# Optimization experiments

Measured on AMD Instinct MI355X. Metric: run time of the kernel, lower is better.

The kernel has to match this reference:

```python
import jax, jax.numpy as jnp
import numpy as np

B, N, DIM = 2, 2048, 1024
HEADS, DIM_HEAD = 16, 64
SOFTCAP = 50.0
ROPE_THETA = 10000.0


def setup_inputs() -> dict:
    key = jax.random.key(0)
    k1, k2, k3 = jax.random.split(key, 3)
    x = jax.random.normal(k1, (B, N, DIM), jnp.float32)
    # structured modality positions: (type, offset, length), non-overlapping, in-bounds
    mods = np.zeros((B, 4, 3), np.int64)
    base_offsets = [200, 700, 1200, 1700]
    for b in range(B):
        for m, o in enumerate(base_offsets):
            mods[b, m] = (0, o + b * 16, 256)
    modalities = jnp.asarray(mods)
    gamma = jnp.zeros((DIM,), jnp.float32)           # RMSNorm gamma (init zeros, used as gamma+1)
    w_qkv = jax.random.normal(k2, (DIM, 3 * HEADS * DIM_HEAD), jnp.float32) * 0.02
    w_out = jax.random.normal(k3, (HEADS * DIM_HEAD, DIM), jnp.float32) * 0.02
    return {"x": x, "modalities": modalities, "gamma": gamma, "w_qkv": w_qkv, "w_out": w_out}


def _rotate_half(x):
    # interleaved-pair rotation, matching rotary-embedding-torch default
    x1, x2 = x[..., 0::2], x[..., 1::2]
    return jnp.stack((-x2, x1), axis=-1).reshape(x.shape)


def reference(x, modalities, gamma, w_qkv, w_out):
    b, n, d = x.shape
    h, dh = HEADS, DIM_HEAD
    seq = jnp.arange(n)
    off = modalities[..., 1]      # [b, m]
    length = modalities[..., 2]   # [b, m]

    # --- modality-aware rotary positions (span interior shrunk by offset [1, -1]) ---
    in_span = (seq[None, None, :] >= (off + 1)[:, :, None]) & (seq[None, None, :] < (off + length)[:, :, None])
    is_any_modality = in_span.any(axis=1)                                   # [b, n]
    pos = (seq[None, :] - jnp.cumsum(is_any_modality.astype(jnp.int32), axis=-1)).astype(jnp.float32)

    # --- RMSNorm: l2norm(x) * sqrt(d) * (gamma + 1) ---
    norm = jnp.maximum(jnp.sqrt(jnp.sum(x * x, axis=-1, keepdims=True)), 1e-12)
    xn = x / norm * jnp.sqrt(jnp.float32(d)) * (gamma + 1.0)

    # --- qkv projection, split heads -> [b, h, n, dh] ---
    qkv = (xn @ w_qkv).reshape(b, n, 3, h, dh)
    q, k, v = jnp.moveaxis(qkv, 2, 0)        # each [b, n, h, dh]
    q = jnp.transpose(q, (0, 2, 1, 3))
    k = jnp.transpose(k, (0, 2, 1, 3))
    v = jnp.transpose(v, (0, 2, 1, 3))

    # --- rotary embedding with modality-aware positions ---
    inv_freq = ROPE_THETA ** (-jnp.arange(0, dh, 2, dtype=jnp.float32) / dh)  # [dh/2]
    ang = pos[:, None, :, None] * inv_freq                                    # [b, 1, n, dh/2]
    ang = jnp.repeat(ang, 2, axis=-1)                                         # [b, 1, n, dh]
    cos, sin = jnp.cos(ang), jnp.sin(ang)
    q = q * cos + _rotate_half(q) * sin
    k = k * cos + _rotate_half(k) * sin

    # --- transfusion attention mask: causal OR per-modality bidirectional span ---
    causal_mask = seq[:, None] >= seq[None, :]                                 # [n, n]
    q_ge = seq[None, None, :] >= off[:, :, None]                               # [b, m, n]
    kv_lt = seq[None, None, :] < (off + length)[:, :, None]                    # [b, m, n]
    mod_mask = (q_ge[:, :, :, None] & kv_lt[:, :, None, :]).any(axis=1)        # [b, n, n]
    mask = causal_mask[None] | mod_mask                                        # [b, n, n]

    # --- attention with softclamp(50) ---
    scale = dh ** -0.5
    sim = jnp.einsum('bhid,bhjd->bhij', q, k) * scale
    sim = jnp.tanh(sim / SOFTCAP) * SOFTCAP
    sim = jnp.where(mask[:, None], sim, jnp.finfo(sim.dtype).min)
    attn = jax.nn.softmax(sim, axis=-1)
    out = jnp.einsum('bhij,bhjd->bhid', attn, v)                               # [b, h, n, dh]
    out = jnp.transpose(out, (0, 2, 1, 3)).reshape(b, n, h * dh)
    return out @ w_out
```

## Files before the change

kernel.cpp:

```cpp
#include <hip/hip_runtime.h>
#include <hip/hip_bf16.h>
#include <stdint.h>

#define B_ 2
#define N_ 2048
#define H_ 16
#define DIM_ 1024
#define NH3 3072
#define ROWS (B_*N_)
#define BHN (B_*H_*N_)

typedef __attribute__((ext_vector_type(8))) short bf16x8;
typedef __attribute__((ext_vector_type(4))) float f32x4;
typedef unsigned short u16;

__device__ __forceinline__ u16 f2bf(float f){
  union { float f; uint32_t u; } v; v.f = f;
  return (u16)((v.u + 0x7fffu + ((v.u >> 16) & 1u)) >> 16);
}

#if __has_builtin(__builtin_amdgcn_exp2f)
#define EXP2F(x) __builtin_amdgcn_exp2f(x)
#else
#define EXP2F(x) __expf((x) * 0.6931471805599453f)
#endif
#if __has_builtin(__builtin_amdgcn_rcpf)
#define RCPF(x) __builtin_amdgcn_rcpf(x)
#else
#define RCPF(x) (1.0f / (x))
#endif

#define GLL16(g, l) __builtin_amdgcn_global_load_lds( \
    (const __attribute__((address_space(1))) void*)(g), \
    (__attribute__((address_space(3))) void*)(l), 16, 0, 0)

__global__ __launch_bounds__(256) void k_prep(
    const float* __restrict__ x, const float* __restrict__ gamma,
    const float* __restrict__ wqkv, const float* __restrict__ wout,
    const int* __restrict__ mods,
    u16* __restrict__ xn, u16* __restrict__ wqkvT, u16* __restrict__ woutT,
    float* __restrict__ cosT, float* __restrict__ sinT)
{
  __shared__ float tile[32][33];
  const int bx = blockIdx.x;
  const int tid = threadIdx.x;
  if (bx < 4096){
    const int row = bx;
    const float4 xv = ((const float4*)(x + (size_t)row*DIM_))[tid];
    float ss = xv.x*xv.x + xv.y*xv.y + xv.z*xv.z + xv.w*xv.w;
#pragma unroll
    for (int d = 1; d < 64; d <<= 1) ss += __shfl_xor(ss, d);
    if ((tid & 63) == 0) tile[1][tid >> 6] = ss;
    __syncthreads();
    float tot = tile[1][0] + tile[1][1] + tile[1][2] + tile[1][3];
    float scl = 32.0f / fmaxf(sqrtf(tot), 1e-12f);
    const float4 gv = ((const float4*)gamma)[tid];
    ushort4 o;
    o.x = f2bf(xv.x * scl * (gv.x + 1.0f));
    o.y = f2bf(xv.y * scl * (gv.y + 1.0f));
    o.z = f2bf(xv.z * scl * (gv.z + 1.0f));
    o.w = f2bf(xv.w * scl * (gv.w + 1.0f));
    ((ushort4*)(xn + (size_t)row*DIM_))[tid] = o;
  } else if (bx < 8192){
    const int t = bx - 4096;
    const int bxx = t & 127, by = t >> 7;
    const float* src; u16* dst; int C, bc;
    if (bxx < 96){ src = wqkv; dst = wqkvT; C = NH3;  bc = bxx*32; }
    else         { src = wout; dst = woutT; C = DIM_; bc = (bxx-96)*32; }
    const int R = DIM_;
    const int tx = tid & 31, ty = tid >> 5;
    const int br = by * 32;
#pragma unroll
    for (int i = 0; i < 32; i += 8)
      tile[ty + i][tx] = src[(size_t)(br + ty + i)*C + bc + tx];
    __syncthreads();
#pragma unroll
    for (int i = 0; i < 32; i += 8)
      dst[(size_t)(bc + ty + i)*R + br + tx] = f2bf(tile[tx][ty + i]);
  } else {
    const int t = (bx - 8192)*256 + tid;
    const int f = t & 31, bn = t >> 5;
    const int b = bn >> 11, n = bn & (N_-1);
    int cum = 0;
#pragma unroll
    for (int m = 0; m < 4; ++m){
      const int off = mods[(b*4 + m)*3 + 1];
      const int len = mods[(b*4 + m)*3 + 2];
      cum += min(max(n - off, 0), len - 1);
    }
    const float pos = (float)(n - cum);
    const float inv = powf(10000.0f, -(float)(2*f) / 64.0f);
    float s, c;
    sincosf(pos * inv, &s, &c);
    cosT[t] = c; sinT[t] = s;
  }
}

template<int MODE, int BM>
__global__ __launch_bounds__(256) void k_gemm(
    const u16* __restrict__ A, const u16* __restrict__ Bt,
    int K, int Nc,
    float* __restrict__ outf,
    const float* __restrict__ cosT, const float* __restrict__ sinT,
    u16* __restrict__ qo, u16* __restrict__ ko, u16* __restrict__ vt)
{
  constexpr int MR = BM/32;
  constexpr int RA = BM/8;
  constexpr int CNT = (RA + 16)/4;
  __shared__ u16 lA[BM*64];
  __shared__ u16 lB[128*64];
  const int tid = threadIdx.x;
  const int wid = tid >> 6, lane = tid & 63;
  const int nx = gridDim.x;
  const int orig = blockIdx.y * nx + blockIdx.x;
  const int qq = (nx * gridDim.y) >> 3;
  const int wgid = (orig & 7) * qq + (orig >> 3);
  const int m0 = (wgid % nx) * BM, n0 = (wgid / nx) * 128;
  const int wm = wid >> 1, wn = wid & 1;
  const int srow = lane >> 3, sch = lane & 7;
  const int r16 = lane & 15, g4 = lane >> 4;
  f32x4 acc[MR][4] = {};
  const int ksteps = K >> 6;
  for (int kt = 0; kt < ksteps; ++kt){
    const int kb = kt*64;
    const int gch = sch ^ srow;
#pragma unroll
    for (int i = 0; i < CNT; ++i){
      const int reg = wid*CNT + i;
      if (reg < RA){
        const int row = reg*8 + srow;
        GLL16(A + (size_t)(m0 + row)*K + kb + gch*8, &lA[reg*512]);
      } else {
        const int r2 = reg - RA;
        const int row = r2*8 + srow;
        GLL16(Bt + (size_t)(n0 + row)*K + kb + gch*8, &lB[r2*512]);
      }
    }
    __syncthreads();
#pragma unroll
    for (int t = 0; t < 2; ++t){
      bf16x8 af[MR], bfr[4];
#pragma unroll
      for (int m = 0; m < MR; ++m){
        int row = wm*(BM/2) + m*16 + r16;
        int ch = (t*4 + g4) ^ (r16 & 7);
        af[m] = *(const bf16x8*)&lA[row*64 + ch*8];
      }
#pragma unroll
      for (int n = 0; n < 4; ++n){
        int row = wn*64 + n*16 + r16;
        int ch = (t*4 + g4) ^ (r16 & 7);
        bfr[n] = *(const bf16x8*)&lB[row*64 + ch*8];
      }
#pragma unroll
      for (int m = 0; m < MR; ++m)
#pragma unroll
        for (int n = 0; n < 4; ++n)
          acc[m][n] = __builtin_amdgcn_mfma_f32_16x16x32_bf16(af[m], bfr[n], acc[m][n], 0, 0, 0);
    }
    __syncthreads();
  }
#pragma unroll
  for (int m = 0; m < MR; ++m){
#pragma unroll
    for (int n = 0; n < 4; ++n){
      if constexpr (MODE == 0){
        const int gcol = n0 + wn*64 + n*16 + r16;
        const int s3 = gcol >> 10, hh = (gcol >> 6) & 15, d = gcol & 63;
        const int grow0 = m0 + wm*(BM/2) + m*16 + g4*4;
        const int b = grow0 >> 11, nn0 = grow0 & (N_-1);
        const size_t hb = (size_t)(b*H_ + hh);
        if (s3 == 2){
          uint32_t w01, w23;
          asm("v_cvt_pk_bf16_f32 %0, %1, %2" : "=v"(w01) : "v"(acc[m][n][0]), "v"(acc[m][n][1]));
          asm("v_cvt_pk_bf16_f32 %0, %1, %2" : "=v"(w23) : "v"(acc[m][n][2]), "v"(acc[m][n][3]));
          *reinterpret_cast<uint2*>(&vt[(hb*64 + d)*N_ + nn0]) = make_uint2(w01, w23);
        } else {
#pragma unroll
          for (int r = 0; r < 4; ++r){
            const float v = acc[m][n][r];
            const float part = __shfl_xor(v, 1);
            const int nn = nn0 + r;
            const int pidx = (b*N_ + nn)*32 + (d >> 1);
            const float c = cosT[pidx], sn = sinT[pidx];
            const float rot = (d & 1) ? (v*c + part*sn) : (v*c - part*sn);
            const u16 val = f2bf(rot);
            if (s3 == 0) qo[(hb*N_ + nn)*64 + d] = val;
            else         ko[(hb*N_ + nn)*64 + d] = val;
          }
        }
      } else {
#pragma unroll
        for (int r = 0; r < 4; ++r){
          const int grow = m0 + wm*(BM/2) + m*16 + g4*4 + r;
          const int gcol = n0 + wn*64 + n*16 + r16;
          outf[(size_t)grow*Nc + gcol] = acc[m][n][r];
        }
      }
    }
  }
}

#define PST 68
__global__ __launch_bounds__(512) void k_attn(
    const u16* __restrict__ qb, const u16* __restrict__ kb, const u16* __restrict__ vt,
    const int* __restrict__ mods, u16* __restrict__ xo)
{
  __shared__ u16 lK[64*64];
  __shared__ u16 lV[64*64];
  __shared__ u16 lP[8*16*PST];
  const int tid = threadIdx.x, wid = tid >> 6, lane = tid & 63;
  const int id = blockIdx.x;
  const int xcd = id & 7, rank = id >> 3;
  const int bh = xcd + 8*(rank & 3);
  const int qslot = rank >> 2;
  const int tp = (qslot < 8) ? (15 - qslot) : (qslot - 8);
  const int b = bh >> 4, h = bh & 15;
  const int r16 = lane & 15, g4 = lane >> 4;
  const int srow = lane >> 3, sch = lane & 7;
  int moff[4], mend[4];
#pragma unroll
  for (int m = 0; m < 4; ++m){
    moff[m] = mods[(b*4+m)*3+1];
    mend[m] = moff[m] + mods[(b*4+m)*3+2];
  }
  const u16* kbase = kb + (size_t)bh*N_*64;
  const u16* vbase = vt + (size_t)bh*64*N_;
  u16* lPw = &lP[wid*16*PST];

  const int q0 = tp*128 + wid*16;
  const int i  = q0 + r16;
  const int imax = tp*128 + 127;
  int jmax = 0, jmax0 = 0;
#pragma unroll
  for (int m = 0; m < 4; ++m){
    if (i  >= moff[m]) jmax  = max(jmax,  mend[m]);
    if (q0 >= moff[m]) jmax0 = max(jmax0, mend[m]);
  }
  const int thrmin = max(q0, jmax0 - 1);
  const u16* qrow = qb + ((size_t)bh*N_ + q0 + r16)*64;
  const bf16x8 aq0 = *(const bf16x8*)&qrow[g4*8];
  const bf16x8 aq1 = *(const bf16x8*)&qrow[32 + g4*8];
  f32x4 o[4] = {};
  f32x4 acc_s = {};
  bf16x8 ones;
#pragma unroll
  for (int j = 0; j < 8; ++j) ones[j] = (short)0x3F80;

  const float D1 = 0.18033688011112043f;
  const float D3 = -3.7570183356483704e-07f;

  for (int kt = 0; kt < N_/64; ++kt){
    bool proc = (kt*64 <= imax);
    if (!proc){
#pragma unroll
      for (int m = 0; m < 4; ++m)
        if (imax >= moff[m] && kt*64 < mend[m]) proc = true;
    }
    if (!proc) continue;
    __syncthreads();
    {
      const int gch = sch ^ srow;
      GLL16(kbase + (size_t)(kt*64 + wid*8 + srow)*64 + gch*8, &lK[wid*512]);
      GLL16(vbase + (size_t)(wid*8 + srow)*N_ + kt*64 + gch*8, &lV[wid*512]);
    }
    __syncthreads();
    f32x4 s[4] = {};
    __builtin_amdgcn_s_setprio(1);
#pragma unroll
    for (int cb = 0; cb < 4; ++cb){
#pragma unroll
      for (int t = 0; t < 2; ++t){
        int row = cb*16 + r16;
        int ch = (t*4 + g4) ^ (row & 7);
        bf16x8 bk = *(const bf16x8*)&lK[row*64 + ch*8];
        s[cb] = __builtin_amdgcn_mfma_f32_16x16x32_bf16(bk, t ? aq1 : aq0, s[cb], 0, 0, 0);
      }
    }
    __builtin_amdgcn_s_setprio(0);
    const int thr = max(i, jmax - 1) - kt*64;
    const bool nomask = (kt*64 + 63 <= thrmin);
#pragma unroll
    for (int cb = 0; cb < 4; ++cb){
      float p[4];
#pragma unroll
      for (int r = 0; r < 4; ++r){
        const float sv = s[cb][r];
        const float w = sv*sv;
        p[r] = EXP2F(sv * fmaf(w, D3, D1));
      }
      if (!nomask){
#pragma unroll
        for (int r = 0; r < 4; ++r)
          p[r] = (cb*16 + g4*4 + r <= thr) ? p[r] : 0.0f;
      }
      uint32_t w01, w23;
      asm("v_cvt_pk_bf16_f32 %0, %1, %2" : "=v"(w01) : "v"(p[0]), "v"(p[1]));
      asm("v_cvt_pk_bf16_f32 %0, %1, %2" : "=v"(w23) : "v"(p[2]), "v"(p[3]));
      *reinterpret_cast<uint2*>(&lPw[r16*PST + cb*16 + g4*4]) = make_uint2(w01, w23);
    }
    asm volatile("s_waitcnt lgkmcnt(0)" ::: "memory");
    __builtin_amdgcn_sched_barrier(0);
    union { uint2 h[2]; bf16x8 v; } u0, u1;
    u0.h[0] = *(const uint2*)&lPw[r16*PST + g4*8];
    u0.h[1] = *(const uint2*)&lPw[r16*PST + g4*8 + 4];
    u1.h[0] = *(const uint2*)&lPw[r16*PST + 32 + g4*8];
    u1.h[1] = *(const uint2*)&lPw[r16*PST + 32 + g4*8 + 4];
    __builtin_amdgcn_s_setprio(1);
    acc_s = __builtin_amdgcn_mfma_f32_16x16x32_bf16(u0.v, ones, acc_s, 0, 0, 0);
    acc_s = __builtin_amdgcn_mfma_f32_16x16x32_bf16(u1.v, ones, acc_s, 0, 0, 0);
#pragma unroll
    for (int cb = 0; cb < 4; ++cb){
#pragma unroll
      for (int t = 0; t < 2; ++t){
        int d = cb*16 + r16;
        int ch = (t*4 + g4) ^ (d & 7);
        bf16x8 bv = *(const bf16x8*)&lV[d*64 + ch*8];
        o[cb] = __builtin_amdgcn_mfma_f32_16x16x32_bf16(t ? u1.v : u0.v, bv, o[cb], 0, 0, 0);
      }
    }
    __builtin_amdgcn_s_setprio(0);
  }
#pragma unroll
  for (int r = 0; r < 4; ++r){
    const float linv = RCPF(acc_s[r]);
    const int iq = q0 + g4*4 + r;
#pragma unroll
    for (int cb = 0; cb < 4; ++cb)
      xo[(size_t)(b*N_ + iq)*DIM_ + h*64 + cb*16 + r16] = f2bf(o[cb][r]*linv);
  }
}

extern "C" void kernel_launch(void* const* d_in, const int* in_sizes, int n_in,
                              void* d_out, int out_size, void* d_ws, size_t ws_size,
                              hipStream_t stream){
  const float* x     = (const float*)d_in[0];
  const int*   mods  = (const int*)d_in[1];
  const float* gamma = (const float*)d_in[2];
  const float* wqkv  = (const float*)d_in[3];
  const float* wout  = (const float*)d_in[4];
  float* outp = (float*)d_out;

  char* p = (char*)d_ws;
  auto alloc = [&](size_t bytes) -> char* {
    char* r = p; p += (bytes + 255) & ~(size_t)255; return r;
  };
  float* cosT  = (float*)alloc((size_t)B_*N_*32*4);
  float* sinT  = (float*)alloc((size_t)B_*N_*32*4);
  u16* wqkvT   = (u16*)alloc((size_t)NH3*DIM_*2);
  u16* woutT   = (u16*)alloc((size_t)DIM_*DIM_*2);
  u16* xn      = (u16*)alloc((size_t)ROWS*DIM_*2);
  u16* qbb     = (u16*)alloc((size_t)BHN*64*2);
  u16* kbb     = (u16*)alloc((size_t)BHN*64*2);
  u16* vtb     = (u16*)alloc((size_t)BHN*64*2);
  u16* xo      = (u16*)alloc((size_t)ROWS*DIM_*2);

  k_prep<<<8704, 256, 0, stream>>>(x, gamma, wqkv, wout, mods, xn, wqkvT, woutT, cosT, sinT);
  k_gemm<0,128><<<dim3(ROWS/128, NH3/128), 256, 0, stream>>>(xn, wqkvT, DIM_, NH3, nullptr, cosT, sinT, qbb, kbb, vtb);
  k_attn<<<512, 512, 0, stream>>>(qbb, kbb, vtb, mods, xo);
  k_gemm<1,64><<<dim3(ROWS/64, DIM_/128), 256, 0, stream>>>(xo, woutT, DIM_, DIM_, outp, nullptr, nullptr, nullptr, nullptr, nullptr);
}
```

Baseline: 115.9 us.

## Give each attention wave two 16-row query tiles to reuse K/V fragments

The attention block shrinks from 8 waves to 4, and each wave now handles 32 query rows as two 16-row halves. Each K and V fragment read from LDS feeds two MFMAs, which halves LDS read traffic per unit of work. Each wave now issues two global-to-LDS loads per tile. The cost is higher register pressure from doubled accumulators and fewer waves per block to hide latency.

Result: slower. 130.5 us (+12.6%).

```diff
diff --git a/kernel.cpp b/kernel.cpp
--- a/kernel.cpp
+++ b/kernel.cpp
@@ -202,13 +202,13 @@
 }
 
 #define PST 68
-__global__ __launch_bounds__(512) void k_attn(
+__global__ __launch_bounds__(256) void k_attn(
     const u16* __restrict__ qb, const u16* __restrict__ kb, const u16* __restrict__ vt,
     const int* __restrict__ mods, u16* __restrict__ xo)
 {
   __shared__ u16 lK[64*64];
   __shared__ u16 lV[64*64];
-  __shared__ u16 lP[8*16*PST];
+  __shared__ u16 lP[4*32*PST];
   const int tid = threadIdx.x, wid = tid >> 6, lane = tid & 63;
   const int id = blockIdx.x;
   const int xcd = id & 7, rank = id >> 3;
@@ -226,23 +226,28 @@
   }
   const u16* kbase = kb + (size_t)bh*N_*64;
   const u16* vbase = vt + (size_t)bh*64*N_;
-  u16* lPw = &lP[wid*16*PST];
-
-  const int q0 = tp*128 + wid*16;
-  const int i  = q0 + r16;
+  u16* lPw = &lP[wid*32*PST];
+
+  const int q0 = tp*128 + wid*32;
+  const int iA = q0 + r16;
+  const int iB = q0 + 16 + r16;
   const int imax = tp*128 + 127;
-  int jmax = 0, jmax0 = 0;
+  int jmaxA = 0, jmaxB = 0, jmax0 = 0;
 #pragma unroll
   for (int m = 0; m < 4; ++m){
-    if (i  >= moff[m]) jmax  = max(jmax,  mend[m]);
+    if (iA >= moff[m]) jmaxA = max(jmaxA, mend[m]);
+    if (iB >= moff[m]) jmaxB = max(jmaxB, mend[m]);
     if (q0 >= moff[m]) jmax0 = max(jmax0, mend[m]);
   }
   const int thrmin = max(q0, jmax0 - 1);
-  const u16* qrow = qb + ((size_t)bh*N_ + q0 + r16)*64;
-  const bf16x8 aq0 = *(const bf16x8*)&qrow[g4*8];
-  const bf16x8 aq1 = *(const bf16x8*)&qrow[32 + g4*8];
-  f32x4 o[4] = {};
-  f32x4 acc_s = {};
+  const u16* qrowA = qb + ((size_t)bh*N_ + iA)*64;
+  const u16* qrowB = qb + ((size_t)bh*N_ + iB)*64;
+  const bf16x8 aqA0 = *(const bf16x8*)&qrowA[g4*8];
+  const bf16x8 aqA1 = *(const bf16x8*)&qrowA[32 + g4*8];
+  const bf16x8 aqB0 = *(const bf16x8*)&qrowB[g4*8];
+  const bf16x8 aqB1 = *(const bf16x8*)&qrowB[32 + g4*8];
+  f32x4 oA[4] = {}, oB[4] = {};
+  f32x4 acc_sA = {}, acc_sB = {};
   bf16x8 ones;
 #pragma unroll
   for (int j = 0; j < 8; ++j) ones[j] = (short)0x3F80;
@@ -261,11 +266,15 @@
     __syncthreads();
     {
       const int gch = sch ^ srow;
-      GLL16(kbase + (size_t)(kt*64 + wid*8 + srow)*64 + gch*8, &lK[wid*512]);
-      GLL16(vbase + (size_t)(wid*8 + srow)*N_ + kt*64 + gch*8, &lV[wid*512]);
-    }
-    __syncthreads();
-    f32x4 s[4] = {};
+#pragma unroll
+      for (int ld = 0; ld < 2; ++ld){
+        const int reg = wid*2 + ld;
+        GLL16(kbase + (size_t)(kt*64 + reg*8 + srow)*64 + gch*8, &lK[reg*512]);
+        GLL16(vbase + (size_t)(reg*8 + srow)*N_ + kt*64 + gch*8, &lV[reg*512]);
+      }
+    }
+    __syncthreads();
+    f32x4 s0[4] = {}, s1[4] = {};
     __builtin_amdgcn_s_setprio(1);
 #pragma unroll
     for (int cb = 0; cb < 4; ++cb){
@@ -274,41 +283,54 @@
         int row = cb*16 + r16;
         int ch = (t*4 + g4) ^ (row & 7);
         bf16x8 bk = *(const bf16x8*)&lK[row*64 + ch*8];
-        s[cb] = __builtin_amdgcn_mfma_f32_16x16x32_bf16(bk, t ? aq1 : aq0, s[cb], 0, 0, 0);
+        s0[cb] = __builtin_amdgcn_mfma_f32_16x16x32_bf16(bk, t ? aqA1 : aqA0, s0[cb], 0, 0, 0);
+        s1[cb] = __builtin_amdgcn_mfma_f32_16x16x32_bf16(bk, t ? aqB1 : aqB0, s1[cb], 0, 0, 0);
       }
     }
     __builtin_amdgcn_s_setprio(0);
-    const int thr = max(i, jmax - 1) - kt*64;
+    const int thrA = max(iA, jmaxA - 1) - kt*64;
+    const int thrB = max(iB, jmaxB - 1) - kt*64;
     const bool nomask = (kt*64 + 63 <= thrmin);
 #pragma unroll
-    for (int cb = 0; cb < 4; ++cb){
-      float p[4];
-#pragma unroll
-      for (int r = 0; r < 4; ++r){
-        const float sv = s[cb][r];
-        const float w = sv*sv;
-        p[r] = EXP2F(sv * fmaf(w, D3, D1));
-      }
-      if (!nomask){
-#pragma unroll
-        for (int r = 0; r < 4; ++r)
-          p[r] = (cb*16 + g4*4 + r <= thr) ? p[r] : 0.0f;
-      }
-      uint32_t w01, w23;
-      asm("v_cvt_pk_bf16_f32 %0, %1, %2" : "=v"(w01) : "v"(p[0]), "v"(p[1]));
-      asm("v_cvt_pk_bf16_f32 %0, %1, %2" : "=v"(w23) : "v"(p[2]), "v"(p[3]));
-      *reinterpret_cast<uint2*>(&lPw[r16*PST + cb*16 + g4*4]) = make_uint2(w01, w23);
+    for (int half = 0; half < 2; ++half){
+      const f32x4* sH = half ? s1 : s0;
+      const int thr = half ? thrB : thrA;
+#pragma unroll
+      for (int cb = 0; cb < 4; ++cb){
+        float p[4];
+#pragma unroll
+        for (int r = 0; r < 4; ++r){
+          const float sv = sH[cb][r];
+          const float w = sv*sv;
+          p[r] = EXP2F(sv * fmaf(w, D3, D1));
+        }
+        if (!nomask){
+#pragma unroll
+          for (int r = 0; r < 4; ++r)
+            p[r] = (cb*16 + g4*4 + r <= thr) ? p[r] : 0.0f;
+        }
+        uint32_t w01, w23;
+        asm("v_cvt_pk_bf16_f32 %0, %1, %2" : "=v"(w01) : "v"(p[0]), "v"(p[1]));
+        asm("v_cvt_pk_bf16_f32 %0, %1, %2" : "=v"(w23) : "v"(p[2]), "v"(p[3]));
+        *reinterpret_cast<uint2*>(&lPw[(half*16 + r16)*PST + cb*16 + g4*4]) = make_uint2(w01, w23);
+      }
     }
     asm volatile("s_waitcnt lgkmcnt(0)" ::: "memory");
     __builtin_amdgcn_sched_barrier(0);
-    union { uint2 h[2]; bf16x8 v; } u0, u1;
-    u0.h[0] = *(const uint2*)&lPw[r16*PST + g4*8];
-    u0.h[1] = *(const uint2*)&lPw[r16*PST + g4*8 + 4];
-    u1.h[0] = *(const uint2*)&lPw[r16*PST + 32 + g4*8];
-    u1.h[1] = *(const uint2*)&lPw[r16*PST + 32 + g4*8 + 4];
+    union { uint2 hh[2]; bf16x8 v; } a0, a1, b0, b1;
+    a0.hh[0] = *(const uint2*)&lPw[r16*PST + g4*8];
+    a0.hh[1] = *(const uint2*)&lPw[r16*PST + g4*8 + 4];
+    a1.hh[0] = *(const uint2*)&lPw[r16*PST + 32 + g4*8];
+    a1.hh[1] = *(const uint2*)&lPw[r16*PST + 32 + g4*8 + 4];
+    b0.hh[0] = *(const uint2*)&lPw[(16 + r16)*PST + g4*8];
+    b0.hh[1] = *(const uint2*)&lPw[(16 + r16)*PST + g4*8 + 4];
+    b1.hh[0] = *(const uint2*)&lPw[(16 + r16)*PST + 32 + g4*8];
+    b1.hh[1] = *(const uint2*)&lPw[(16 + r16)*PST + 32 + g4*8 + 4];
     __builtin_amdgcn_s_setprio(1);
-    acc_s = __builtin_amdgcn_mfma_f32_16x16x32_bf16(u0.v, ones, acc_s, 0, 0, 0);
-    acc_s = __builtin_amdgcn_mfma_f32_16x16x32_bf16(u1.v, ones, acc_s, 0, 0, 0);
+    acc_sA = __builtin_amdgcn_mfma_f32_16x16x32_bf16(a0.v, ones, acc_sA, 0, 0, 0);
+    acc_sA = __builtin_amdgcn_mfma_f32_16x16x32_bf16(a1.v, ones, acc_sA, 0, 0, 0);
+    acc_sB = __builtin_amdgcn_mfma_f32_16x16x32_bf16(b0.v, ones, acc_sB, 0, 0, 0);
+    acc_sB = __builtin_amdgcn_mfma_f32_16x16x32_bf16(b1.v, ones, acc_sB, 0, 0, 0);
 #pragma unroll
     for (int cb = 0; cb < 4; ++cb){
 #pragma unroll
@@ -316,18 +338,23 @@
         int d = cb*16 + r16;
         int ch = (t*4 + g4) ^ (d & 7);
         bf16x8 bv = *(const bf16x8*)&lV[d*64 + ch*8];
-        o[cb] = __builtin_amdgcn_mfma_f32_16x16x32_bf16(t ? u1.v : u0.v, bv, o[cb], 0, 0, 0);
+        oA[cb] = __builtin_amdgcn_mfma_f32_16x16x32_bf16(t ? a1.v : a0.v, bv, oA[cb], 0, 0, 0);
+        oB[cb] = __builtin_amdgcn_mfma_f32_16x16x32_bf16(t ? b1.v : b0.v, bv, oB[cb], 0, 0, 0);
       }
     }
     __builtin_amdgcn_s_setprio(0);
   }
 #pragma unroll
   for (int r = 0; r < 4; ++r){
-    const float linv = RCPF(acc_s[r]);
-    const int iq = q0 + g4*4 + r;
-#pragma unroll
-    for (int cb = 0; cb < 4; ++cb)
-      xo[(size_t)(b*N_ + iq)*DIM_ + h*64 + cb*16 + r16] = f2bf(o[cb][r]*linv);
+    const float linvA = RCPF(acc_sA[r]);
+    const float linvB = RCPF(acc_sB[r]);
+    const int iqA = q0 + g4*4 + r;
+    const int iqB = q0 + 16 + g4*4 + r;
+#pragma unroll
+    for (int cb = 0; cb < 4; ++cb){
+      xo[(size_t)(b*N_ + iqA)*DIM_ + h*64 + cb*16 + r16] = f2bf(oA[cb][r]*linvA);
+      xo[(size_t)(b*N_ + iqB)*DIM_ + h*64 + cb*16 + r16] = f2bf(oB[cb][r]*linvB);
+    }
   }
 }
 
@@ -357,6 +384,6 @@
 
   k_prep<<<8704, 256, 0, stream>>>(x, gamma, wqkv, wout, mods, xn, wqkvT, woutT, cosT, sinT);
   k_gemm<0,128><<<dim3(ROWS/128, NH3/128), 256, 0, stream>>>(xn, wqkvT, DIM_, NH3, nullptr, cosT, sinT, qbb, kbb, vtb);
-  k_attn<<<512, 512, 0, stream>>>(qbb, kbb, vtb, mods, xo);
+  k_attn<<<512, 256, 0, stream>>>(qbb, kbb, vtb, mods, xo);
   k_gemm<1,64><<<dim3(ROWS/64, DIM_/128), 256, 0, stream>>>(xo, woutT, DIM_, DIM_, outp, nullptr, nullptr, nullptr, nullptr, nullptr);
 }
```

## Switch attention to 32x32 MFMA with register-resident P via permlane swap

Applied to the files above, without the earlier changes.

Rewrites the attention inner loop to use 32x32x16 bf16 MFMA tiles, so each of 4 waves handles 32 query rows instead of 8 waves each handling 16. The P matrix is kept in registers and rearranged with v_permlane32_swap instead of a round trip through LDS, and the row sum is accumulated in scalar registers instead of a ones-matrix MFMA. This aims to remove LDS traffic, the waitcnt barrier and extra MFMA work per tile. The cost is higher register pressure and half the threads per block, which lowers occupancy and latency hiding.

New measurement: 128.9 us. 1.11x slower.

```diff
diff --git a/kernel.cpp b/kernel.cpp
--- a/kernel.cpp
+++ b/kernel.cpp
@@ -12,6 +12,7 @@
 
 typedef __attribute__((ext_vector_type(8))) short bf16x8;
 typedef __attribute__((ext_vector_type(4))) float f32x4;
+typedef __attribute__((ext_vector_type(16))) float f32x16;
 typedef unsigned short u16;
 
 __device__ __forceinline__ u16 f2bf(float f){
@@ -201,14 +202,12 @@
   }
 }
 
-#define PST 68
-__global__ __launch_bounds__(512) void k_attn(
+__global__ __launch_bounds__(256) void k_attn(
     const u16* __restrict__ qb, const u16* __restrict__ kb, const u16* __restrict__ vt,
     const int* __restrict__ mods, u16* __restrict__ xo)
 {
   __shared__ u16 lK[64*64];
   __shared__ u16 lV[64*64];
-  __shared__ u16 lP[8*16*PST];
   const int tid = threadIdx.x, wid = tid >> 6, lane = tid & 63;
   const int id = blockIdx.x;
   const int xcd = id & 7, rank = id >> 3;
@@ -216,7 +215,7 @@
   const int qslot = rank >> 2;
   const int tp = (qslot < 8) ? (15 - qslot) : (qslot - 8);
   const int b = bh >> 4, h = bh & 15;
-  const int r16 = lane & 15, g4 = lane >> 4;
+  const int l31 = lane & 31, hi = lane >> 5;
   const int srow = lane >> 3, sch = lane & 7;
   int moff[4], mend[4];
 #pragma unroll
@@ -226,26 +225,26 @@
   }
   const u16* kbase = kb + (size_t)bh*N_*64;
   const u16* vbase = vt + (size_t)bh*64*N_;
-  u16* lPw = &lP[wid*16*PST];
-
-  const int q0 = tp*128 + wid*16;
-  const int i  = q0 + r16;
+
+  const int q0w = tp*128 + wid*32;
+  const int qG  = q0w + l31;
   const int imax = tp*128 + 127;
   int jmax = 0, jmax0 = 0;
 #pragma unroll
   for (int m = 0; m < 4; ++m){
-    if (i  >= moff[m]) jmax  = max(jmax,  mend[m]);
-    if (q0 >= moff[m]) jmax0 = max(jmax0, mend[m]);
-  }
-  const int thrmin = max(q0, jmax0 - 1);
-  const u16* qrow = qb + ((size_t)bh*N_ + q0 + r16)*64;
-  const bf16x8 aq0 = *(const bf16x8*)&qrow[g4*8];
-  const bf16x8 aq1 = *(const bf16x8*)&qrow[32 + g4*8];
-  f32x4 o[4] = {};
-  f32x4 acc_s = {};
-  bf16x8 ones;
-#pragma unroll
-  for (int j = 0; j < 8; ++j) ones[j] = (short)0x3F80;
+    if (qG  >= moff[m]) jmax  = max(jmax,  mend[m]);
+    if (q0w >= moff[m]) jmax0 = max(jmax0, mend[m]);
+  }
+  const int thrg = max(qG, jmax - 1);
+  const int thrmin = max(q0w, jmax0 - 1);
+  const u16* qrow = qb + ((size_t)bh*N_ + qG)*64;
+  bf16x8 qf[4];
+#pragma unroll
+  for (int t = 0; t < 4; ++t)
+    qf[t] = *(const bf16x8*)&qrow[t*16 + hi*8];
+
+  f32x16 o0 = {}, o1 = {};
+  float lsum = 0.f;
 
   const float D1 = 0.18033688011112043f;
   const float D3 = -3.7570183356483704e-07f;
@@ -261,73 +260,83 @@
     __syncthreads();
     {
       const int gch = sch ^ srow;
-      GLL16(kbase + (size_t)(kt*64 + wid*8 + srow)*64 + gch*8, &lK[wid*512]);
-      GLL16(vbase + (size_t)(wid*8 + srow)*N_ + kt*64 + gch*8, &lV[wid*512]);
-    }
-    __syncthreads();
-    f32x4 s[4] = {};
+#pragma unroll
+      for (int ld = 0; ld < 2; ++ld){
+        const int reg = wid*2 + ld;
+        GLL16(kbase + (size_t)(kt*64 + reg*8 + srow)*64 + gch*8, &lK[reg*512]);
+        GLL16(vbase + (size_t)(reg*8 + srow)*N_ + kt*64 + gch*8, &lV[reg*512]);
+      }
+    }
+    __syncthreads();
+    f32x16 s0 = {}, s1 = {};
     __builtin_amdgcn_s_setprio(1);
 #pragma unroll
-    for (int cb = 0; cb < 4; ++cb){
-#pragma unroll
-      for (int t = 0; t < 2; ++t){
-        int row = cb*16 + r16;
-        int ch = (t*4 + g4) ^ (row & 7);
-        bf16x8 bk = *(const bf16x8*)&lK[row*64 + ch*8];
-        s[cb] = __builtin_amdgcn_mfma_f32_16x16x32_bf16(bk, t ? aq1 : aq0, s[cb], 0, 0, 0);
-      }
+    for (int t = 0; t < 4; ++t){
+      const int c = t*2 + hi;
+      const int r0 = l31, r1 = 32 + l31;
+      const bf16x8 k0 = *(const bf16x8*)&lK[r0*64 + (c ^ (r0 & 7))*8];
+      const bf16x8 k1 = *(const bf16x8*)&lK[r1*64 + (c ^ (r1 & 7))*8];
+      s0 = __builtin_amdgcn_mfma_f32_32x32x16_bf16(k0, qf[t], s0, 0, 0, 0);
+      s1 = __builtin_amdgcn_mfma_f32_32x32x16_bf16(k1, qf[t], s1, 0, 0, 0);
     }
     __builtin_amdgcn_s_setprio(0);
-    const int thr = max(i, jmax - 1) - kt*64;
+    const int thr = thrg - kt*64;
     const bool nomask = (kt*64 + 63 <= thrmin);
-#pragma unroll
-    for (int cb = 0; cb < 4; ++cb){
-      float p[4];
-#pragma unroll
-      for (int r = 0; r < 4; ++r){
-        const float sv = s[cb][r];
+    float p0[16], p1[16];
+#pragma unroll
+    for (int reg = 0; reg < 16; ++reg){
+      const int kb32 = (reg & 3) + 8*(reg >> 2);
+      {
+        const float sv = s0[reg];
         const float w = sv*sv;
-        p[r] = EXP2F(sv * fmaf(w, D3, D1));
-      }
-      if (!nomask){
-#pragma unroll
-        for (int r = 0; r < 4; ++r)
-          p[r] = (cb*16 + g4*4 + r <= thr) ? p[r] : 0.0f;
-      }
-      uint32_t w01, w23;
-      asm("v_cvt_pk_bf16_f32 %0, %1, %2" : "=v"(w01) : "v"(p[0]), "v"(p[1]));
-      asm("v_cvt_pk_bf16_f32 %0, %1, %2" : "=v"(w23) : "v"(p[2]), "v"(p[3]));
-      *reinterpret_cast<uint2*>(&lPw[r16*PST + cb*16 + g4*4]) = make_uint2(w01, w23);
-    }
-    asm volatile("s_waitcnt lgkmcnt(0)" ::: "memory");
-    __builtin_amdgcn_sched_barrier(0);
-    union { uint2 h[2]; bf16x8 v; } u0, u1;
-    u0.h[0] = *(const uint2*)&lPw[r16*PST + g4*8];
-    u0.h[1] = *(const uint2*)&lPw[r16*PST + g4*8 + 4];
-    u1.h[0] = *(const uint2*)&lPw[r16*PST + 32 + g4*8];
-    u1.h[1] = *(const uint2*)&lPw[r16*PST + 32 + g4*8 + 4];
+        float p = EXP2F(sv * fmaf(w, D3, D1));
+        if (!nomask) p = (kb32 + 4*hi <= thr) ? p : 0.0f;
+        p0[reg] = p; lsum += p;
+      }
+      {
+        const float sv = s1[reg];
+        const float w = sv*sv;
+        float p = EXP2F(sv * fmaf(w, D3, D1));
+        if (!nomask) p = (32 + kb32 + 4*hi <= thr) ? p : 0.0f;
+        p1[reg] = p; lsum += p;
+      }
+    }
+    bf16x8 pf[4];
+#pragma unroll
+    for (int ks = 0; ks < 4; ++ks){
+      const float* pp = (ks < 2) ? p0 : p1;
+      const int q32 = ks & 1;
+      uint32_t X0, X1, Y0, Y1;
+      asm("v_cvt_pk_bf16_f32 %0, %1, %2" : "=v"(X0) : "v"(pp[q32*8+0]), "v"(pp[q32*8+1]));
+      asm("v_cvt_pk_bf16_f32 %0, %1, %2" : "=v"(X1) : "v"(pp[q32*8+2]), "v"(pp[q32*8+3]));
+      asm("v_cvt_pk_bf16_f32 %0, %1, %2" : "=v"(Y0) : "v"(pp[q32*8+4]), "v"(pp[q32*8+5]));
+      asm("v_cvt_pk_bf16_f32 %0, %1, %2" : "=v"(Y1) : "v"(pp[q32*8+6]), "v"(pp[q32*8+7]));
+      asm volatile("v_permlane32_swap_b32 %0, %1" : "+v"(X0), "+v"(Y0));
+      asm volatile("v_permlane32_swap_b32 %0, %1" : "+v"(X1), "+v"(Y1));
+      union { uint32_t d[4]; bf16x8 v; } u;
+      u.d[0] = X0; u.d[1] = X1; u.d[2] = Y0; u.d[3] = Y1;
+      pf[ks] = u.v;
+    }
     __builtin_amdgcn_s_setprio(1);
-    acc_s = __builtin_amdgcn_mfma_f32_16x16x32_bf16(u0.v, ones, acc_s, 0, 0, 0);
-    acc_s = __builtin_amdgcn_mfma_f32_16x16x32_bf16(u1.v, ones, acc_s, 0, 0, 0);
-#pragma unroll
-    for (int cb = 0; cb < 4; ++cb){
-#pragma unroll
-      for (int t = 0; t < 2; ++t){
-        int d = cb*16 + r16;
-        int ch = (t*4 + g4) ^ (d & 7);
-        bf16x8 bv = *(const bf16x8*)&lV[d*64 + ch*8];
-        o[cb] = __builtin_amdgcn_mfma_f32_16x16x32_bf16(t ? u1.v : u0.v, bv, o[cb], 0, 0, 0);
-      }
+#pragma unroll
+    for (int ks = 0; ks < 4; ++ks){
+      const int d0 = l31, d1 = 32 + l31;
+      const int c = ks*2 + hi;
+      const bf16x8 v0 = *(const bf16x8*)&lV[d0*64 + (c ^ (d0 & 7))*8];
+      const bf16x8 v1 = *(const bf16x8*)&lV[d1*64 + (c ^ (d1 & 7))*8];
+      o0 = __builtin_amdgcn_mfma_f32_32x32x16_bf16(pf[ks], v0, o0, 0, 0, 0);
+      o1 = __builtin_amdgcn_mfma_f32_32x32x16_bf16(pf[ks], v1, o1, 0, 0, 0);
     }
     __builtin_amdgcn_s_setprio(0);
   }
-#pragma unroll
-  for (int r = 0; r < 4; ++r){
-    const float linv = RCPF(acc_s[r]);
-    const int iq = q0 + g4*4 + r;
-#pragma unroll
-    for (int cb = 0; cb < 4; ++cb)
-      xo[(size_t)(b*N_ + iq)*DIM_ + h*64 + cb*16 + r16] = f2bf(o[cb][r]*linv);
+  lsum += __shfl_xor(lsum, 32);
+#pragma unroll
+  for (int reg = 0; reg < 16; ++reg){
+    const int q_loc = (reg & 3) + 8*(reg >> 2) + 4*hi;
+    const float linv = RCPF(__shfl(lsum, q_loc));
+    const int iq = q0w + q_loc;
+    xo[(size_t)(b*N_ + iq)*DIM_ + h*64 + l31]      = f2bf(o0[reg]*linv);
+    xo[(size_t)(b*N_ + iq)*DIM_ + h*64 + 32 + l31] = f2bf(o1[reg]*linv);
   }
 }
 
@@ -357,6 +366,6 @@
 
   k_prep<<<8704, 256, 0, stream>>>(x, gamma, wqkv, wout, mods, xn, wqkvT, woutT, cosT, sinT);
   k_gemm<0,128><<<dim3(ROWS/128, NH3/128), 256, 0, stream>>>(xn, wqkvT, DIM_, NH3, nullptr, cosT, sinT, qbb, kbb, vtb);
-  k_attn<<<512, 512, 0, stream>>>(qbb, kbb, vtb, mods, xo);
+  k_attn<<<512, 256, 0, stream>>>(qbb, kbb, vtb, mods, xo);
   k_gemm<1,64><<<dim3(ROWS/64, DIM_/128), 256, 0, stream>>>(xo, woutT, DIM_, DIM_, outp, nullptr, nullptr, nullptr, nullptr, nullptr);
 }
```
